# Optimization experiments

Measured on AMD Instinct MI355X. Metric: run time of the kernel, lower is better.

Reference implementation:

```python
import jax, jax.numpy as jnp
import numpy as np

DIM = 1024
MLP_MULT = 4
NUM_EXPERTS = 8
EXPERT_HIDDEN = MLP_MULT * DIM // NUM_EXPERTS  # 512


def setup_inputs() -> dict:
    key = jax.random.key(0)
    k_x, k_r, k_fc, k_pj = jax.random.split(key, 4)
    x = jax.random.normal(k_x, (4, 4096, DIM), dtype=jnp.float32)
    # router: nn.Linear(dim, num_experts, bias=False) -> weight [E, D]
    w_router = jax.random.normal(k_r, (NUM_EXPERTS, DIM), dtype=jnp.float32) * (1.0 / np.sqrt(DIM))
    # per-expert fc: Linear(dim, hidden) weight [H, D]; stacked [E, H, D]
    w_fc = jax.random.normal(k_fc, (NUM_EXPERTS, EXPERT_HIDDEN, DIM), dtype=jnp.float32) * (1.0 / np.sqrt(DIM))
    # per-expert proj: Linear(hidden, dim) weight [D, H]; stacked [E, D, H]
    # (_zero_init in the original; use small random values so the reference output is non-trivial)
    w_proj = jax.random.normal(k_pj, (NUM_EXPERTS, DIM, EXPERT_HIDDEN), dtype=jnp.float32) * (1.0 / np.sqrt(EXPERT_HIDDEN))
    return {"x": x, "w_router": w_router, "w_fc": w_fc, "w_proj": w_proj}


def reference(x, w_router, w_fc, w_proj):
    # Router on detached input; top-1 expert per token.
    logits = jnp.einsum('bsd,ed->bse', jax.lax.stop_gradient(x), w_router)
    weights = jax.nn.softmax(logits, axis=-1)  # computed as in original (unused in output)
    indices = jnp.argmax(weights, axis=-1)     # [B, S]
    onehot = jax.nn.one_hot(indices, NUM_EXPERTS, dtype=x.dtype)  # [B, S, E]
    # Dense dispatch: run all experts, combine with one-hot (equivalent to mask gather/scatter).
    h = jnp.einsum('bsd,ehd->bseh', x, w_fc)              # [B, S, E, H]
    h = jnp.where(h >= 0, h, 0.5 * h)                      # leaky_relu(negative_slope=0.5)
    h = h * h                                              # square
    out = jnp.einsum('bseh,edh,bse->bsd', h, w_proj, onehot)
    return out
```

## Files before the change

kernel.cpp:

```cpp
#include <hip/hip_runtime.h>
#include <stdint.h>
#include <stddef.h>

#define DIM 1024
#define NEXP 8
#define HID 512
#define NTOK 16384
#define NB_HIST 64
#define NB_ROUTER 1024
#define NB_CAST 512

typedef __attribute__((ext_vector_type(4))) float f32x4;
typedef __attribute__((ext_vector_type(8))) short short8;
typedef __attribute__((ext_vector_type(2))) unsigned int u32x2;
typedef __attribute__((ext_vector_type(4))) unsigned int u32x4;

__device__ __forceinline__ unsigned short f2b(float f) {
  unsigned int u = __float_as_uint(f);
  return (unsigned short)((u + 0x7FFFu + ((u >> 16) & 1u)) >> 16);
}

__device__ __forceinline__ unsigned int pk_bf16(float a, float b) {
  unsigned int r;
  asm volatile("v_cvt_pk_bf16_f32 %0, %1, %2" : "=v"(r) : "v"(a), "v"(b));
  return r;
}

__device__ __forceinline__ void gload_lds16(const void* g, void* l) {
  __builtin_amdgcn_global_load_lds((const __attribute__((address_space(1))) void*)g,
                                   (__attribute__((address_space(3))) void*)l, 16, 0, 0);
}

__global__ __launch_bounds__(256) void k_router_cast(
    const float* __restrict__ x, const float* __restrict__ wr,
    int* __restrict__ eid,
    const float* __restrict__ wfc, const float* __restrict__ wpj,
    unsigned short* __restrict__ oa, unsigned short* __restrict__ ob) {
  int bid = blockIdx.x;
  if (bid < NB_ROUTER) {
    int w = threadIdx.x >> 6, lane = threadIdx.x & 63;
    int t0 = bid * 16 + w * 4;
    const float* xr = x + (size_t)t0 * DIM;
    float s[4][NEXP];
#pragma unroll
    for (int j = 0; j < 4; j++)
#pragma unroll
      for (int e = 0; e < NEXP; e++) s[j][e] = 0.f;
#pragma unroll
    for (int i = 0; i < 4; i++) {
      f32x4 xv[4];
#pragma unroll
      for (int j = 0; j < 4; j++) xv[j] = *(const f32x4*)(xr + j * DIM + lane * 4 + 256 * i);
#pragma unroll
      for (int e = 0; e < NEXP; e++) {
        f32x4 wv = *(const f32x4*)(wr + e * DIM + lane * 4 + 256 * i);
#pragma unroll
        for (int j = 0; j < 4; j++)
          s[j][e] += xv[j].x * wv.x + xv[j].y * wv.y + xv[j].z * wv.z + xv[j].w * wv.w;
      }
    }
#pragma unroll
    for (int j = 0; j < 4; j++)
#pragma unroll
      for (int e = 0; e < NEXP; e++) {
        float v = s[j][e];
#pragma unroll
        for (int off = 32; off > 0; off >>= 1) v += __shfl_xor(v, off);
        s[j][e] = v;
      }
    if (lane == 0) {
#pragma unroll
      for (int j = 0; j < 4; j++) {
        int be = 0;
        float bv = s[j][0];
#pragma unroll
        for (int e = 1; e < NEXP; e++) {
          if (s[j][e] > bv) { bv = s[j][e]; be = e; }
        }
        eid[t0 + j] = be;
      }
    }
  } else {
    const int n4 = NEXP * HID * DIM / 4;
    int stride = NB_CAST * 256;
    for (int i = (bid - NB_ROUTER) * 256 + (int)threadIdx.x; i < n4; i += stride) {
      f32x4 va = ((const f32x4*)wfc)[i];
      f32x4 vb = ((const f32x4*)wpj)[i];
      u32x2 ua, ub;
      ua.x = pk_bf16(va.x, va.y); ua.y = pk_bf16(va.z, va.w);
      ub.x = pk_bf16(vb.x, vb.y); ub.y = pk_bf16(vb.z, vb.w);
      ((u32x2*)oa)[i] = ua;
      ((u32x2*)ob)[i] = ub;
    }
  }
}

__global__ __launch_bounds__(256) void k_hist(const int* __restrict__ eid,
                                              int* __restrict__ bc) {
  __shared__ int h[NEXP];
  if (threadIdx.x < NEXP) h[threadIdx.x] = 0;
  __syncthreads();
  int tok = blockIdx.x * (NTOK / NB_HIST) + threadIdx.x;
  atomicAdd(&h[eid[tok]], 1);
  __syncthreads();
  if (threadIdx.x < NEXP) bc[blockIdx.x * NEXP + threadIdx.x] = h[threadIdx.x];
}

__global__ void k_scan(const int* __restrict__ bc, int* __restrict__ offs,
                       int* __restrict__ base) {
  __shared__ int cnt[NEXP];
  __shared__ int so[NEXP + 1];
  int t = threadIdx.x;
  if (t < NEXP) {
    int run = 0;
    for (int b = 0; b < NB_HIST; b++) {
      base[b * NEXP + t] = run;
      run += bc[b * NEXP + t];
    }
    cnt[t] = run;
  }
  __syncthreads();
  if (t == 0) {
    int a = 0;
    for (int e = 0; e < NEXP; e++) { so[e] = a; a += cnt[e]; }
    so[NEXP] = a;
  }
  __syncthreads();
  if (t < NEXP + 1) offs[t] = so[t];
  for (int i = t; i < NB_HIST * NEXP; i += blockDim.x) base[i] += so[i % NEXP];
}

__global__ __launch_bounds__(256) void k_scatter(const int* __restrict__ eid,
                                                 const int* __restrict__ base,
                                                 int* __restrict__ tlist) {
  __shared__ int cur[NEXP];
  if (threadIdx.x < NEXP) cur[threadIdx.x] = base[blockIdx.x * NEXP + threadIdx.x];
  __syncthreads();
  int tok = blockIdx.x * (NTOK / NB_HIST) + threadIdx.x;
  int e = eid[tok];
  int pos = atomicAdd(&cur[e], 1);
  tlist[pos] = tok;
}

__device__ __forceinline__ bool tile_map_g(const int* offs, int NB, int bid, int G,
                                           int& e, int& mb, int& nb) {
  int l = (bid & 7) * (G >> 3) + (bid >> 3);
  e = -1; mb = 0; nb = 0;
  int acc2 = 0;
#pragma unroll
  for (int i = 0; i < NEXP; i++) {
    int mi = offs[i + 1] - offs[i];
    int tb = ((mi + 127) >> 7) * NB;
    if (e < 0 && l < acc2 + tb) {
      int r = l - acc2;
      e = i; mb = r / NB; nb = r % NB;
    }
    acc2 += tb;
  }
  return e >= 0;
}

__global__ __launch_bounds__(256) void k_gemm_fc(
    const float* __restrict__ x, const unsigned short* __restrict__ wb,
    const int* __restrict__ offs, const int* __restrict__ tlist,
    unsigned short* __restrict__ hout) {
  constexpr int KDIM = DIM, NDIM = HID;
  int e, mb, nb;
  if (!tile_map_g(offs, 4, (int)blockIdx.x, (int)gridDim.x, e, mb, nb)) return;
  int off = offs[e], me = offs[e + 1] - off, m0 = mb * 128, n0 = nb * 128;

  __shared__ unsigned short As[3][128 * 32];
  __shared__ unsigned short Bs[3][128 * 32];

  int t = threadIdx.x, lane = t & 63, w = t >> 6;
  int wm = w >> 1, wn = w & 1;

  int kb = (lane & 3) ^ ((lane >> 3) & 3);

  const unsigned short* bsrc[2];
  const float* af32[2];
#pragma unroll
  for (int i = 0; i < 2; i++) {
    int r = i * 64 + w * 16 + (lane >> 2);
    bsrc[i] = wb + ((size_t)e * NDIM + n0 + r) * (size_t)KDIM + kb * 8;
    int gm = m0 + r;
    if (gm > me - 1) gm = me - 1;
    af32[i] = x + (size_t)tlist[off + gm] * DIM + kb * 8;
  }
  int awoff0 = (w * 16) * 32 + lane * 8;
  int awoff1 = (64 + w * 16) * 32 + lane * 8;

  f32x4 acc[4][4] = {};
  constexpr int NT = KDIM / 32;

  unsigned short* a0 = &As[0][0]; unsigned short* b0 = &Bs[0][0];
  unsigned short* a1 = &As[1][0]; unsigned short* b1 = &Bs[1][0];
  unsigned short* a2 = &As[2][0]; unsigned short* b2 = &Bs[2][0];

  f32x4 r00, r01, r10, r11;

#define ISSUE_A(kt_)                                              \
  do {                                                            \
    r00 = *(const f32x4*)(af32[0] + (kt_) * 32);                  \
    r01 = *(const f32x4*)(af32[0] + (kt_) * 32 + 4);              \
    r10 = *(const f32x4*)(af32[1] + (kt_) * 32);                  \
    r11 = *(const f32x4*)(af32[1] + (kt_) * 32 + 4);              \
  } while (0)
#define ISSUE_B(kt_, db_)                                         \
  do {                                                            \
    gload_lds16(bsrc[0] + (kt_) * 32, (db_) + (w * 16) * 32);     \
    gload_lds16(bsrc[1] + (kt_) * 32, (db_) + (64 + w * 16) * 32);\
  } while (0)
#define WRITE_A(da_)                                              \
  do {                                                            \
    u32x4 c0, c1;                                                 \
    c0.x = pk_bf16(r00.x, r00.y); c0.y = pk_bf16(r00.z, r00.w);   \
    c0.z = pk_bf16(r01.x, r01.y); c0.w = pk_bf16(r01.z, r01.w);   \
    c1.x = pk_bf16(r10.x, r10.y); c1.y = pk_bf16(r10.z, r10.w);   \
    c1.z = pk_bf16(r11.x, r11.y); c1.w = pk_bf16(r11.z, r11.w);   \
    *(u32x4*)&(da_)[awoff0] = c0;                                 \
    *(u32x4*)&(da_)[awoff1] = c1;                                 \
  } while (0)

  ISSUE_A(0);
  ISSUE_B(0, b0);
  ISSUE_B(1, b1);

  for (int kt = 0; kt < NT; kt++) {
    if (kt == NT - 1) {
      asm volatile("s_waitcnt vmcnt(0)" ::: "memory");
    } else {
      asm volatile("s_waitcnt vmcnt(2)" ::: "memory");
    }
    __builtin_amdgcn_sched_barrier(0);
    WRITE_A(a0);
    asm volatile("s_waitcnt lgkmcnt(0)" ::: "memory");
    __builtin_amdgcn_sched_barrier(0);
    __builtin_amdgcn_s_barrier();
    if (kt + 1 < NT) ISSUE_A(kt + 1);
    if (kt + 2 < NT) ISSUE_B(kt + 2, b2);

    short8 af[4], bf[4];
#pragma unroll
    for (int i = 0; i < 4; i++) {
      int ra = wm * 64 + i * 16 + (lane & 15);
      int ca = (lane >> 4) ^ ((ra >> 1) & 3);
      af[i] = *(const short8*)&a0[ra * 32 + ca * 8];
      int rbb = wn * 64 + i * 16 + (lane & 15);
      int cb = (lane >> 4) ^ ((rbb >> 1) & 3);
      bf[i] = *(const short8*)&b0[rbb * 32 + cb * 8];
    }
    __builtin_amdgcn_s_setprio(1);
#pragma unroll
    for (int mi = 0; mi < 4; mi++)
#pragma unroll
      for (int ni = 0; ni < 4; ni++)
        acc[mi][ni] =
            __builtin_amdgcn_mfma_f32_16x16x32_bf16(af[mi], bf[ni], acc[mi][ni], 0, 0, 0);
    __builtin_amdgcn_s_setprio(0);

    unsigned short* ta = a0; a0 = a1; a1 = a2; a2 = ta;
    unsigned short* tb = b0; b0 = b1; b1 = b2; b2 = tb;
  }
#undef ISSUE_A
#undef ISSUE_B
#undef WRITE_A

  int rb = (lane >> 4) * 4, cb = lane & 15;
#pragma unroll
  for (int mi = 0; mi < 4; mi++) {
#pragma unroll
    for (int j = 0; j < 4; j++) {
      int ml = wm * 64 + mi * 16 + rb + j;
      if (m0 + ml < me) {
#pragma unroll
        for (int ni = 0; ni < 4; ni++) {
          int col = n0 + wn * 64 + ni * 16 + cb;
          float v = acc[mi][ni][j];
          v = (v >= 0.f) ? v * v : 0.25f * v * v;
          hout[(size_t)(off + m0 + ml) * HID + col] = f2b(v);
        }
      }
    }
  }
}

__global__ __launch_bounds__(256) void k_gemm_pj(
    const unsigned short* __restrict__ hin, const unsigned short* __restrict__ wb,
    const int* __restrict__ offs, const int* __restrict__ tlist,
    float* __restrict__ out) {
  constexpr int KDIM = HID, NDIM = DIM;
  int e, mb, nb;
  if (!tile_map_g(offs, 8, (int)blockIdx.x, (int)gridDim.x, e, mb, nb)) return;
  int off = offs[e], me = offs[e + 1] - off, m0 = mb * 128, n0 = nb * 128;

  __shared__ unsigned short lds[3][2][128 * 32];

  int t = threadIdx.x, lane = t & 63, w = t >> 6;
  int wm = w >> 1, wn = w & 1;

  int kb = (lane & 3) ^ ((lane >> 3) & 3);

  const unsigned short* asrc[2];
  const unsigned short* bsrc[2];
#pragma unroll
  for (int i = 0; i < 2; i++) {
    int r = i * 64 + w * 16 + (lane >> 2);
    int gm = m0 + r;
    if (gm > me - 1) gm = me - 1;
    asrc[i] = hin + (size_t)(off + gm) * KDIM + kb * 8;
    bsrc[i] = wb + ((size_t)e * NDIM + n0 + r) * (size_t)KDIM + kb * 8;
  }

  f32x4 acc[4][4] = {};
  constexpr int NT = KDIM / 32;

  unsigned short* b0a = &lds[0][0][0]; unsigned short* b0b = &lds[0][1][0];
  unsigned short* b1a = &lds[1][0][0]; unsigned short* b1b = &lds[1][1][0];
  unsigned short* b2a = &lds[2][0][0]; unsigned short* b2b = &lds[2][1][0];

#define STAGE(kt_, da_, db_)                                       \
  do {                                                             \
    gload_lds16(asrc[0] + (kt_) * 32, (da_) + (w * 16) * 32);      \
    gload_lds16(asrc[1] + (kt_) * 32, (da_) + (64 + w * 16) * 32); \
    gload_lds16(bsrc[0] + (kt_) * 32, (db_) + (w * 16) * 32);      \
    gload_lds16(bsrc[1] + (kt_) * 32, (db_) + (64 + w * 16) * 32); \
  } while (0)

  STAGE(0, b0a, b0b);
  STAGE(1, b1a, b1b);

  for (int kt = 0; kt < NT; kt++) {
    if (kt < NT - 1) {
      asm volatile("s_waitcnt vmcnt(4)" ::: "memory");
    } else {
      asm volatile("s_waitcnt vmcnt(0)" ::: "memory");
    }
    __builtin_amdgcn_s_barrier();

    if (kt + 2 < NT) STAGE(kt + 2, b2a, b2b);

    short8 af[4], bf[4];
#pragma unroll
    for (int i = 0; i < 4; i++) {
      int ra = wm * 64 + i * 16 + (lane & 15);
      int ca = (lane >> 4) ^ ((ra >> 1) & 3);
      af[i] = *(const short8*)&b0a[ra * 32 + ca * 8];
      int rbb = wn * 64 + i * 16 + (lane & 15);
      int cb = (lane >> 4) ^ ((rbb >> 1) & 3);
      bf[i] = *(const short8*)&b0b[rbb * 32 + cb * 8];
    }
    __builtin_amdgcn_s_setprio(1);
#pragma unroll
    for (int mi = 0; mi < 4; mi++)
#pragma unroll
      for (int ni = 0; ni < 4; ni++)
        acc[mi][ni] =
            __builtin_amdgcn_mfma_f32_16x16x32_bf16(af[mi], bf[ni], acc[mi][ni], 0, 0, 0);
    __builtin_amdgcn_s_setprio(0);

    unsigned short* ta = b0a; b0a = b1a; b1a = b2a; b2a = ta;
    unsigned short* tb = b0b; b0b = b1b; b1b = b2b; b2b = tb;
  }
#undef STAGE

  int rb = (lane >> 4) * 4, cb = lane & 15;
#pragma unroll
  for (int mi = 0; mi < 4; mi++) {
#pragma unroll
    for (int j = 0; j < 4; j++) {
      int ml = wm * 64 + mi * 16 + rb + j;
      if (m0 + ml < me) {
        int tok = tlist[off + m0 + ml];
#pragma unroll
        for (int ni = 0; ni < 4; ni++) {
          int col = n0 + wn * 64 + ni * 16 + cb;
          out[(size_t)tok * DIM + col] = acc[mi][ni][j];
        }
      }
    }
  }
}

extern "C" void kernel_launch(void* const* d_in, const int* in_sizes, int n_in,
                              void* d_out, int out_size, void* d_ws, size_t ws_size,
                              hipStream_t stream) {
  const float* x = (const float*)d_in[0];
  const float* wr = (const float*)d_in[1];
  const float* wfc = (const float*)d_in[2];
  const float* wpj = (const float*)d_in[3];
  float* out = (float*)d_out;

  uintptr_t p = (uintptr_t)d_ws;
  int* offs = (int*)p;  p += 256;
  int* bc = (int*)p;    p += sizeof(int) * NB_HIST * NEXP;
  int* base = (int*)p;  p += sizeof(int) * NB_HIST * NEXP;
  int* eid = (int*)p;   p += sizeof(int) * NTOK;
  int* tlist = (int*)p; p += sizeof(int) * NTOK;
  unsigned short* wfc_b = (unsigned short*)p; p += (size_t)NEXP * HID * DIM * 2;
  unsigned short* wpj_b = (unsigned short*)p; p += (size_t)NEXP * DIM * HID * 2;
  unsigned short* hbuf = (unsigned short*)p;  p += (size_t)NTOK * HID * 2;

  k_router_cast<<<NB_ROUTER + NB_CAST, 256, 0, stream>>>(
      x, wr, eid, wfc, wpj, wfc_b, wpj_b);
  k_hist<<<NB_HIST, 256, 0, stream>>>(eid, bc);
  k_scan<<<1, 256, 0, stream>>>(bc, offs, base);
  k_scatter<<<NB_HIST, 256, 0, stream>>>(eid, base, tlist);
  k_gemm_fc<<<dim3(544), 256, 0, stream>>>(x, wfc_b, offs, tlist, hbuf);
  k_gemm_pj<<<dim3(1080), 256, 0, stream>>>(hbuf, wpj_b, offs, tlist, out);
}
```

Baseline: 104.7 us.

## Enlarge projection GEMM tiles to 256x256 with 512 threads and interleaved staging

```diff
diff --git a/kernel.cpp b/kernel.cpp
--- a/kernel.cpp
+++ b/kernel.cpp
@@ -285,91 +285,124 @@
   }
 }
 
-__global__ __launch_bounds__(256) void k_gemm_pj(
+__global__ __launch_bounds__(512) void k_gemm_pj(
     const unsigned short* __restrict__ hin, const unsigned short* __restrict__ wb,
     const int* __restrict__ offs, const int* __restrict__ tlist,
     float* __restrict__ out) {
-  constexpr int KDIM = HID, NDIM = DIM;
-  int e, mb, nb;
-  if (!tile_map_g(offs, 8, (int)blockIdx.x, (int)gridDim.x, e, mb, nb)) return;
-  int off = offs[e], me = offs[e + 1] - off, m0 = mb * 128, n0 = nb * 128;
-
-  __shared__ unsigned short lds[3][2][128 * 32];
-
-  int t = threadIdx.x, lane = t & 63, w = t >> 6;
-  int wm = w >> 1, wn = w & 1;
-
-  int kb = (lane & 3) ^ ((lane >> 3) & 3);
-
-  const unsigned short* asrc[2];
-  const unsigned short* bsrc[2];
-#pragma unroll
-  for (int i = 0; i < 2; i++) {
-    int r = i * 64 + w * 16 + (lane >> 2);
+  int e = -1, mb = 0, nb = 0;
+  {
+    int l = ((int)blockIdx.x & 7) * ((int)gridDim.x >> 3) + ((int)blockIdx.x >> 3);
+    int acc2 = 0;
+#pragma unroll
+    for (int i = 0; i < NEXP; i++) {
+      int mi = offs[i + 1] - offs[i];
+      int tb = ((mi + 255) >> 8) * 4;
+      if (e < 0 && l < acc2 + tb) { int r = l - acc2; e = i; mb = r >> 2; nb = r & 3; }
+      acc2 += tb;
+    }
+  }
+  if (e < 0) return;
+  int off = offs[e], me = offs[e + 1] - off, m0 = mb * 256, n0 = nb * 256;
+
+  __shared__ unsigned short As[2][256 * 64];
+  __shared__ unsigned short Bs[2][256 * 64];
+
+  int t = threadIdx.x;
+  int lane = t & 63, wid = t >> 6;
+  int wm = wid >> 2, wn = wid & 3;
+
+  int gsw = (t & 7) ^ ((t >> 4) & 7);
+  const unsigned short* ap[4];
+  const unsigned short* bp0 = wb + ((size_t)e * DIM + n0 + (t >> 3)) * (size_t)HID + gsw * 8;
+#pragma unroll
+  for (int p = 0; p < 4; p++) {
+    int r = p * 64 + (t >> 3);
     int gm = m0 + r;
     if (gm > me - 1) gm = me - 1;
-    asrc[i] = hin + (size_t)(off + gm) * KDIM + kb * 8;
-    bsrc[i] = wb + ((size_t)e * NDIM + n0 + r) * (size_t)KDIM + kb * 8;
-  }
-
-  f32x4 acc[4][4] = {};
-  constexpr int NT = KDIM / 32;
-
-  unsigned short* b0a = &lds[0][0][0]; unsigned short* b0b = &lds[0][1][0];
-  unsigned short* b1a = &lds[1][0][0]; unsigned short* b1b = &lds[1][1][0];
-  unsigned short* b2a = &lds[2][0][0]; unsigned short* b2b = &lds[2][1][0];
-
-#define STAGE(kt_, da_, db_)                                       \
-  do {                                                             \
-    gload_lds16(asrc[0] + (kt_) * 32, (da_) + (w * 16) * 32);      \
-    gload_lds16(asrc[1] + (kt_) * 32, (da_) + (64 + w * 16) * 32); \
-    gload_lds16(bsrc[0] + (kt_) * 32, (db_) + (w * 16) * 32);      \
-    gload_lds16(bsrc[1] + (kt_) * 32, (db_) + (64 + w * 16) * 32); \
+    ap[p] = hin + (size_t)(off + gm) * HID + gsw * 8;
+  }
+  int sdst = t * 8;
+
+  int swr = (lane & 15) >> 1;
+  f32x4 acc[8][4] = {};
+
+#define PSTG_A(kt_, d_, p_) \
+  gload_lds16(ap[p_] + (kt_) * 64, &As[d_][(p_) * 4096 + sdst])
+#define PSTG_B(kt_, d_, p_) \
+  gload_lds16(bp0 + (size_t)(p_) * 64 * HID + (kt_) * 64, &Bs[d_][(p_) * 4096 + sdst])
+
+#define PJ_QUAD(q_, Ad_)                                                        \
+  do {                                                                          \
+    short8 afr[2][2];                                                           \
+    _Pragma("unroll") for (int ii = 0; ii < 2; ii++)                            \
+      _Pragma("unroll") for (int ks = 0; ks < 2; ks++) {                        \
+        int ra = wm * 128 + (2 * (q_) + ii) * 16 + (lane & 15);                 \
+        int slot = (ks * 4 + (lane >> 4)) ^ swr;                                \
+        afr[ii][ks] = *(const short8*)&(Ad_)[ra * 64 + slot * 8];               \
+      }                                                                         \
+    __builtin_amdgcn_s_setprio(1);                                              \
+    _Pragma("unroll") for (int ii = 0; ii < 2; ii++)                            \
+      _Pragma("unroll") for (int ni = 0; ni < 4; ni++)                          \
+        _Pragma("unroll") for (int ks = 0; ks < 2; ks++)                        \
+          acc[2 * (q_) + ii][ni] = __builtin_amdgcn_mfma_f32_16x16x32_bf16(     \
+              afr[ii][ks], breg[ni][ks], acc[2 * (q_) + ii][ni], 0, 0, 0);      \
+    __builtin_amdgcn_s_setprio(0);                                              \
   } while (0)
 
-  STAGE(0, b0a, b0b);
-  STAGE(1, b1a, b1b);
-
-  for (int kt = 0; kt < NT; kt++) {
-    if (kt < NT - 1) {
+  constexpr int NKT = HID / 64;
+
+  PSTG_B(0, 0, 0); PSTG_B(0, 0, 1); PSTG_B(0, 0, 2); PSTG_B(0, 0, 3);
+  PSTG_A(0, 0, 0); PSTG_A(0, 0, 2); PSTG_A(0, 0, 1); PSTG_A(0, 0, 3);
+
+  for (int kt = 0; kt < NKT; kt++) {
+    int d = kt & 1;
+    const unsigned short* Ad = &As[d][0];
+    const unsigned short* Bd = &Bs[d][0];
+    bool more = (kt + 1) < NKT;
+
+    asm volatile("s_waitcnt vmcnt(2)" ::: "memory");
+    __builtin_amdgcn_s_barrier();
+
+    short8 breg[4][2];
+#pragma unroll
+    for (int ni = 0; ni < 4; ni++)
+#pragma unroll
+      for (int ks = 0; ks < 2; ks++) {
+        int rbB = wn * 64 + ni * 16 + (lane & 15);
+        int slot = (ks * 4 + (lane >> 4)) ^ swr;
+        breg[ni][ks] = *(const short8*)&Bd[rbB * 64 + slot * 8];
+      }
+    if (more) { PSTG_B(kt + 1, d ^ 1, 0); PSTG_B(kt + 1, d ^ 1, 1); }
+    PJ_QUAD(0, Ad);
+    __builtin_amdgcn_s_barrier();
+
+    if (more) { PSTG_B(kt + 1, d ^ 1, 2); PSTG_B(kt + 1, d ^ 1, 3); }
+    PJ_QUAD(1, Ad);
+    __builtin_amdgcn_s_barrier();
+
+    if (more) {
       asm volatile("s_waitcnt vmcnt(4)" ::: "memory");
     } else {
       asm volatile("s_waitcnt vmcnt(0)" ::: "memory");
     }
     __builtin_amdgcn_s_barrier();
-
-    if (kt + 2 < NT) STAGE(kt + 2, b2a, b2b);
-
-    short8 af[4], bf[4];
-#pragma unroll
-    for (int i = 0; i < 4; i++) {
-      int ra = wm * 64 + i * 16 + (lane & 15);
-      int ca = (lane >> 4) ^ ((ra >> 1) & 3);
-      af[i] = *(const short8*)&b0a[ra * 32 + ca * 8];
-      int rbb = wn * 64 + i * 16 + (lane & 15);
-      int cb = (lane >> 4) ^ ((rbb >> 1) & 3);
-      bf[i] = *(const short8*)&b0b[rbb * 32 + cb * 8];
-    }
-    __builtin_amdgcn_s_setprio(1);
-#pragma unroll
-    for (int mi = 0; mi < 4; mi++)
-#pragma unroll
-      for (int ni = 0; ni < 4; ni++)
-        acc[mi][ni] =
-            __builtin_amdgcn_mfma_f32_16x16x32_bf16(af[mi], bf[ni], acc[mi][ni], 0, 0, 0);
-    __builtin_amdgcn_s_setprio(0);
-
-    unsigned short* ta = b0a; b0a = b1a; b1a = b2a; b2a = ta;
-    unsigned short* tb = b0b; b0b = b1b; b1b = b2b; b2b = tb;
-  }
-#undef STAGE
-
-  int rb = (lane >> 4) * 4, cb = lane & 15;
-#pragma unroll
-  for (int mi = 0; mi < 4; mi++) {
+    if (more) { PSTG_A(kt + 1, d ^ 1, 0); PSTG_A(kt + 1, d ^ 1, 2); }
+    PJ_QUAD(2, Ad);
+    __builtin_amdgcn_s_barrier();
+
+    if (more) { PSTG_A(kt + 1, d ^ 1, 1); PSTG_A(kt + 1, d ^ 1, 3); }
+    PJ_QUAD(3, Ad);
+  }
+#undef PSTG_A
+#undef PSTG_B
+#undef PJ_QUAD
+
+  int rbase = (lane >> 4) * 4, cb = lane & 15;
+#pragma unroll
+  for (int mi = 0; mi < 8; mi++) {
 #pragma unroll
     for (int j = 0; j < 4; j++) {
-      int ml = wm * 64 + mi * 16 + rb + j;
+      int ml = wm * 128 + mi * 16 + rbase + j;
       if (m0 + ml < me) {
         int tok = tlist[off + m0 + ml];
 #pragma unroll
@@ -407,5 +440,5 @@
   k_scan<<<1, 256, 0, stream>>>(bc, offs, base);
   k_scatter<<<NB_HIST, 256, 0, stream>>>(eid, base, tlist);
   k_gemm_fc<<<dim3(544), 256, 0, stream>>>(x, wfc_b, offs, tlist, hbuf);
-  k_gemm_pj<<<dim3(1080), 256, 0, stream>>>(hbuf, wpj_b, offs, tlist, out);
-}
+  k_gemm_pj<<<dim3(288), 512, 0, stream>>>(hbuf, wpj_b, offs, tlist, out);
+}
```

Measured after the change: 128.6 us. 22.8% more time.
